# Kernel tuning notes

Measured on AMD Instinct MI355X. Metric: run time of the kernel, lower is better.

Reference implementation:

```python
import jax, jax.numpy as jnp
import numpy as np

N, C, T, V = 128, 64, 128, 25   # batch, channels (in==out), frames, joints
R = 8                            # rel_channels = in_channels // rel_reduction
H = 12                           # SE hidden dim for joint attention (~V//2)


def setup_inputs() -> dict:
    key = jax.random.key(0)
    ks = jax.random.split(key, 8)
    w = lambda shape, k: jax.random.normal(k, shape, jnp.float32) * 0.05
    return {
        "x": jax.random.normal(ks[0], (N, C, T, V), jnp.float32),
        "A": jax.random.normal(ks[1], (V, V), jnp.float32) * 0.1,
        "w1": w((R, C), ks[2]), "b1": jnp.zeros((R,), jnp.float32),
        "w2": w((R, C), ks[3]), "b2": jnp.zeros((R,), jnp.float32),
        "w4": w((C, R), ks[4]), "b4": jnp.zeros((C,), jnp.float32),
        "se_w1": w((H, V), ks[5]), "se_b1": jnp.zeros((H,), jnp.float32),
        "se_w2": w((V, H), ks[6]), "se_b2": jnp.zeros((V,), jnp.float32),
    }


def reference(x, A, w1, b1, w2, b2, w4, b4, se_w1, se_b1, se_w2, se_b2):
    alpha = 1.0
    # conv1/conv2 are 1x1 convs; mean over T commutes with the linear map,
    # so pool first then project (saves a (N,R,T,V) intermediate).
    xm = x.mean(axis=2)                                     # (N,C,V)
    x1 = jnp.einsum('rc,ncv->nrv', w1, xm) + b1[None, :, None]
    x2 = jnp.einsum('rc,ncv->nrv', w2, xm) + b2[None, :, None]
    # channel-wise relation: broadcast diff + tanh  -> (N,R,V,V)
    rel = jnp.tanh(x1[:, :, :, None] - x2[:, :, None, :])
    # conv4 (1x1) lifts R->C, scale by alpha, add static adjacency
    Adyn = jnp.einsum('or,nruv->nouv', w4, rel) + b4[None, :, None, None]
    Adyn = Adyn * alpha + A[None, None]                     # (N,C,V,V)
    # DRJointSpa: SE attention over joints (pool C,T -> FC -> ReLU -> FC -> sigmoid)
    s = x.mean(axis=(1, 2))                                 # (N,V)
    h = jax.nn.relu(jnp.einsum('hv,nv->nh', se_w1, s) + se_b1)
    a = jax.nn.sigmoid(jnp.einsum('vh,nh->nv', se_w2, h) + se_b2)
    x3 = x * a[:, None, None, :]                            # (N,C,T,V)
    # per-channel graph aggregation over joints
    return jnp.einsum('ncuv,nctv->nctu', Adyn, x3)
```

## Files before the change

### kernel.cpp

```cpp
#include <hip/hip_runtime.h>
#include <hip/hip_bf16.h>

#define NN 128
#define CC 64
#define TT 128
#define VV 25
#define RR 8
#define HH 12
#define TPAD 132

__global__ __launch_bounds__(256) void kA_tmean(const float* __restrict__ x,
                                                float* __restrict__ xm) {
    const int blk = blockIdx.x;
    const int tid = threadIdx.x;
    __shared__ float st[TT * VV];
    __shared__ float ps[8 * VV];

    const float4* xb4 = (const float4*)(x + (size_t)blk * (TT * VV));
    float4* st4 = (float4*)st;
    for (int i = tid; i < (TT * VV) / 4; i += 256) st4[i] = xb4[i];
    __syncthreads();

    if (tid < 200) {
        const int v = tid % VV, tseg = tid / VV;
        float s = 0.f;
        const int base = tseg * 16 * VV + v;
#pragma unroll
        for (int i = 0; i < 16; i++) s += st[base + i * VV];
        ps[tseg * VV + v] = s;
    }
    __syncthreads();
    if (tid < VV) {
        float s = 0.f;
#pragma unroll
        for (int k = 0; k < 8; k++) s += ps[k * VV + tid];
        xm[(size_t)blk * VV + tid] = s * (1.f / TT);
    }
}

__global__ __launch_bounds__(256) void kB_small(
    const float* __restrict__ xm,
    const float* __restrict__ w1, const float* __restrict__ b1,
    const float* __restrict__ w2, const float* __restrict__ b2,
    const float* __restrict__ sw1, const float* __restrict__ sb1,
    const float* __restrict__ sw2, const float* __restrict__ sb2,
    float* __restrict__ a_out, float* __restrict__ rel_out) {
    const int n = blockIdx.x;
    const int tid = threadIdx.x;
    __shared__ float lxm[CC * VV];
    __shared__ float ls[VV];
    __shared__ float lh[HH];
    __shared__ float l1[RR * VV];
    __shared__ float l2[RR * VV];

    for (int i = tid; i < CC * VV; i += 256) lxm[i] = xm[(size_t)n * CC * VV + i];
    __syncthreads();

    if (tid < VV) {
        float s = 0.f;
        for (int c = 0; c < CC; c++) s += lxm[c * VV + tid];
        ls[tid] = s * (1.f / CC);
    }
    if (tid < RR * VV) {
        int r = tid / VV, v = tid % VV;
        float s1 = b1[r], s2 = b2[r];
        for (int c = 0; c < CC; c++) {
            float xv = lxm[c * VV + v];
            s1 += w1[r * CC + c] * xv;
            s2 += w2[r * CC + c] * xv;
        }
        l1[tid] = s1;
        l2[tid] = s2;
    }
    __syncthreads();

    if (tid < HH) {
        float h = sb1[tid];
        for (int v = 0; v < VV; v++) h += sw1[tid * VV + v] * ls[v];
        lh[tid] = fmaxf(h, 0.f);
    }
    __syncthreads();

    if (tid < VV) {
        float z = sb2[tid];
        for (int j = 0; j < HH; j++) z += sw2[tid * HH + j] * lh[j];
        a_out[(size_t)n * VV + tid] = 1.f / (1.f + expf(-z));
    }

    for (int idx = tid; idx < RR * VV * VV; idx += 256) {
        int r = idx / (VV * VV);
        int rem = idx % (VV * VV);
        int u = rem / VV, v = rem % VV;
        rel_out[(size_t)n * RR * VV * VV + idx] = tanhf(l1[r * VV + u] - l2[r * VV + v]);
    }
}

__global__ __launch_bounds__(256) void kC_main(
    const float* __restrict__ x, const float* __restrict__ A,
    const float* __restrict__ w4, const float* __restrict__ b4,
    const float* __restrict__ rel, const float* __restrict__ av,
    float* __restrict__ out) {
    const int blk = blockIdx.x;
    const int n = blk / CC;
    const int c = blk % CC;
    const int tid = threadIdx.x;

    __shared__ float ad[28 * 28];
    __shared__ float xs[28 * TPAD];
    float* os = xs;

    float w4r[RR];
#pragma unroll
    for (int r = 0; r < RR; r++) w4r[r] = w4[c * RR + r];
    const float b4c = b4[c];

    for (int uv = tid; uv < 28 * 28; uv += 256) {
        int u = uv / 28, v = uv % 28;
        float val = 0.f;
        if (u < VV && v < VV) {
            val = b4c + A[u * VV + v];
            const float* rp = rel + (size_t)n * RR * VV * VV + u * VV + v;
#pragma unroll
            for (int r = 0; r < RR; r++) val += w4r[r] * rp[r * VV * VV];
            val *= av[(size_t)n * VV + v];
        }
        ad[uv] = val;
    }

    const float4* xb4 = (const float4*)(x + (size_t)blk * (TT * VV));
    for (int i = tid; i < (TT * VV) / 4; i += 256) {
        float4 q = xb4[i];
        int lin = i * 4;
        float vals[4] = {q.x, q.y, q.z, q.w};
#pragma unroll
        for (int k = 0; k < 4; k++) {
            int l = lin + k;
            int t = l / VV, v = l - t * VV;
            xs[v * TPAD + t] = vals[k];
        }
    }
    for (int i = tid; i < 3 * TPAD; i += 256) xs[25 * TPAD + i] = 0.f;
    __syncthreads();

    const int ug = tid >> 5;
    const int tg = tid & 31;
    const int u0 = ug * 4;
    const int t0 = tg * 4;
    float acc[4][4];
#pragma unroll
    for (int dt = 0; dt < 4; dt++)
#pragma unroll
        for (int j = 0; j < 4; j++) acc[dt][j] = 0.f;

    if (ug < 7) {
#pragma unroll
        for (int vb = 0; vb < 7; vb++) {
            float4 a4[4];
            float4 x4[4];
#pragma unroll
            for (int j = 0; j < 4; j++) a4[j] = *(const float4*)&ad[(u0 + j) * 28 + vb * 4];
#pragma unroll
            for (int vi = 0; vi < 4; vi++) x4[vi] = *(const float4*)&xs[(vb * 4 + vi) * TPAD + t0];
            const float* xv = (const float*)&x4[0];
#pragma unroll
            for (int dt = 0; dt < 4; dt++) {
#pragma unroll
                for (int j = 0; j < 4; j++) {
                    acc[dt][j] += a4[j].x * xv[0 * 4 + dt];
                    acc[dt][j] += a4[j].y * xv[1 * 4 + dt];
                    acc[dt][j] += a4[j].z * xv[2 * 4 + dt];
                    acc[dt][j] += a4[j].w * xv[3 * 4 + dt];
                }
            }
        }
    }
    __syncthreads();

    if (ug < 7) {
#pragma unroll
        for (int dt = 0; dt < 4; dt++) {
#pragma unroll
            for (int j = 0; j < 4; j++) {
                int u = u0 + j;
                if (u < VV) os[(t0 + dt) * VV + u] = acc[dt][j];
            }
        }
    }
    __syncthreads();

    float4* ob4 = (float4*)(out + (size_t)blk * (TT * VV));
    const float4* os4 = (const float4*)os;
    for (int i = tid; i < (TT * VV) / 4; i += 256) ob4[i] = os4[i];
}

extern "C" void kernel_launch(void* const* d_in, const int* in_sizes, int n_in,
                              void* d_out, int out_size, void* d_ws, size_t ws_size,
                              hipStream_t stream) {
    const float* x   = (const float*)d_in[0];
    const float* A   = (const float*)d_in[1];
    const float* w1  = (const float*)d_in[2];
    const float* b1  = (const float*)d_in[3];
    const float* w2  = (const float*)d_in[4];
    const float* b2  = (const float*)d_in[5];
    const float* w4  = (const float*)d_in[6];
    const float* b4  = (const float*)d_in[7];
    const float* sw1 = (const float*)d_in[8];
    const float* sb1 = (const float*)d_in[9];
    const float* sw2 = (const float*)d_in[10];
    const float* sb2 = (const float*)d_in[11];
    float* out = (float*)d_out;

    float* ws = (float*)d_ws;
    float* xm  = ws;
    float* a_s = xm + (size_t)NN * CC * VV;
    float* rel = a_s + (size_t)NN * VV;

    kA_tmean<<<NN * CC, 256, 0, stream>>>(x, xm);
    kB_small<<<NN, 256, 0, stream>>>(xm, w1, b1, w2, b2, sw1, sb1, sw2, sb2, a_s, rel);
    kC_main<<<NN * CC, 256, 0, stream>>>(x, A, w4, b4, rel, a_s, out);
}
```

Before: 248.7 us.

## Precompute per-(n,c) dynamic adjacency in small kernel, load it in main kernel

Moves construction of the scaled dynamic adjacency (w4·rel + b4 + A, times joint attention) out of the main aggregation kernel and into the middle kernel. That kernel now runs two blocks per sample, keeps rel in shared memory, and writes a padded 28x28 adjacency per (n,c) to workspace. The main kernel then only does a float4 load of its adjacency tile instead of eight strided rel reads plus FMAs per element. This adds about 25 MB of workspace traffic and a middle kernel with only 256 blocks, each doing a serial 32-channel loop.

```diff
diff --git a/kernel.cpp b/kernel.cpp
--- a/kernel.cpp
+++ b/kernel.cpp
@@ -8,6 +8,7 @@
 #define RR 8
 #define HH 12
 #define TPAD 132
+#define ADSZ 784
 
 __global__ __launch_bounds__(256) void kA_tmean(const float* __restrict__ x,
                                                 float* __restrict__ xm) {
@@ -38,22 +39,33 @@
     }
 }
 
-__global__ __launch_bounds__(256) void kB_small(
-    const float* __restrict__ xm,
+__global__ __launch_bounds__(256) void kB2_adbuild(
+    const float* __restrict__ xm, const float* __restrict__ A,
     const float* __restrict__ w1, const float* __restrict__ b1,
     const float* __restrict__ w2, const float* __restrict__ b2,
+    const float* __restrict__ w4, const float* __restrict__ b4,
     const float* __restrict__ sw1, const float* __restrict__ sb1,
     const float* __restrict__ sw2, const float* __restrict__ sb2,
-    float* __restrict__ a_out, float* __restrict__ rel_out) {
-    const int n = blockIdx.x;
+    float* __restrict__ ad_ws) {
+    const int n = blockIdx.x >> 1;
+    const int chalf = blockIdx.x & 1;
     const int tid = threadIdx.x;
+
     __shared__ float lxm[CC * VV];
+    __shared__ float lA[VV * VV];
+    __shared__ float lw4[CC * RR];
+    __shared__ float lb4[CC];
     __shared__ float ls[VV];
     __shared__ float lh[HH];
+    __shared__ float la[VV];
     __shared__ float l1[RR * VV];
     __shared__ float l2[RR * VV];
+    __shared__ float lrel[RR * VV * VV];
 
     for (int i = tid; i < CC * VV; i += 256) lxm[i] = xm[(size_t)n * CC * VV + i];
+    for (int i = tid; i < VV * VV; i += 256) lA[i] = A[i];
+    for (int i = tid; i < CC * RR; i += 256) lw4[i] = w4[i];
+    if (tid < CC) lb4[tid] = b4[tid];
     __syncthreads();
 
     if (tid < VV) {
@@ -84,48 +96,55 @@
     if (tid < VV) {
         float z = sb2[tid];
         for (int j = 0; j < HH; j++) z += sw2[tid * HH + j] * lh[j];
-        a_out[(size_t)n * VV + tid] = 1.f / (1.f + expf(-z));
-    }
-
+        la[tid] = 1.f / (1.f + expf(-z));
+    }
     for (int idx = tid; idx < RR * VV * VV; idx += 256) {
         int r = idx / (VV * VV);
         int rem = idx % (VV * VV);
         int u = rem / VV, v = rem % VV;
-        rel_out[(size_t)n * RR * VV * VV + idx] = tanhf(l1[r * VV + u] - l2[r * VV + v]);
+        lrel[idx] = tanhf(l1[r * VV + u] - l2[r * VV + v]);
+    }
+    __syncthreads();
+
+    if (tid < ADSZ / 4) {
+        const int c0 = chalf * 32;
+        for (int ci = 0; ci < 32; ci++) {
+            const int c = c0 + ci;
+            const float b4c = lb4[c];
+            const float* w4c = &lw4[c * RR];
+            float4 q;
+            float* qe = (float*)&q;
+#pragma unroll
+            for (int k = 0; k < 4; k++) {
+                int uv = tid * 4 + k;
+                int u = uv / 28, v = uv - u * 28;
+                float val = 0.f;
+                if (u < VV && v < VV) {
+                    int e = u * VV + v;
+                    val = b4c + lA[e];
+#pragma unroll
+                    for (int r = 0; r < RR; r++) val += w4c[r] * lrel[r * VV * VV + e];
+                    val *= la[v];
+                }
+                qe[k] = val;
+            }
+            ((float4*)(ad_ws + ((size_t)n * CC + c) * ADSZ))[tid] = q;
+        }
     }
 }
 
 __global__ __launch_bounds__(256) void kC_main(
-    const float* __restrict__ x, const float* __restrict__ A,
-    const float* __restrict__ w4, const float* __restrict__ b4,
-    const float* __restrict__ rel, const float* __restrict__ av,
+    const float* __restrict__ x, const float* __restrict__ ad_ws,
     float* __restrict__ out) {
     const int blk = blockIdx.x;
-    const int n = blk / CC;
-    const int c = blk % CC;
     const int tid = threadIdx.x;
 
-    __shared__ float ad[28 * 28];
+    __shared__ float ad[ADSZ];
     __shared__ float xs[28 * TPAD];
     float* os = xs;
 
-    float w4r[RR];
-#pragma unroll
-    for (int r = 0; r < RR; r++) w4r[r] = w4[c * RR + r];
-    const float b4c = b4[c];
-
-    for (int uv = tid; uv < 28 * 28; uv += 256) {
-        int u = uv / 28, v = uv % 28;
-        float val = 0.f;
-        if (u < VV && v < VV) {
-            val = b4c + A[u * VV + v];
-            const float* rp = rel + (size_t)n * RR * VV * VV + u * VV + v;
-#pragma unroll
-            for (int r = 0; r < RR; r++) val += w4r[r] * rp[r * VV * VV];
-            val *= av[(size_t)n * VV + v];
-        }
-        ad[uv] = val;
-    }
+    if (tid < ADSZ / 4)
+        ((float4*)ad)[tid] = ((const float4*)(ad_ws + (size_t)blk * ADSZ))[tid];
 
     const float4* xb4 = (const float4*)(x + (size_t)blk * (TT * VV));
     for (int i = tid; i < (TT * VV) / 4; i += 256) {
@@ -211,11 +230,11 @@
     float* out = (float*)d_out;
 
     float* ws = (float*)d_ws;
-    float* xm  = ws;
-    float* a_s = xm + (size_t)NN * CC * VV;
-    float* rel = a_s + (size_t)NN * VV;
+    float* ad_ws = ws;
+    float* xm    = ad_ws + (size_t)NN * CC * ADSZ;
 
     kA_tmean<<<NN * CC, 256, 0, stream>>>(x, xm);
-    kB_small<<<NN, 256, 0, stream>>>(xm, w1, b1, w2, b2, sw1, sb1, sw2, sb2, a_s, rel);
-    kC_main<<<NN * CC, 256, 0, stream>>>(x, A, w4, b4, rel, a_s, out);
-}
+    kB2_adbuild<<<NN * 2, 256, 0, stream>>>(xm, A, w1, b1, w2, b2, w4, b4,
+                                            sw1, sb1, sw2, sb2, ad_ws);
+    kC_main<<<NN * CC, 256, 0, stream>>>(x, ad_ws, out);
+}
```

Result: slower. 256.1 us (+3.0%).
